# Kernel tuning notes

Hardware: AMD Instinct MI355X
Metric: run time of the kernel (lower is better)

Reference implementation:

```python
import jax, jax.numpy as jnp
import numpy as np

DIM = 2048
NUM_HEADS = 16
HEAD_DIM = DIM // NUM_HEADS
ROPE_BASE = 10000.0


def _rope_cos_sin(seq_len, head_dim, dtype):
    inv_freq = 1.0 / (ROPE_BASE ** (jnp.arange(0, head_dim, 2, dtype=jnp.float32) / head_dim))
    t = jnp.arange(seq_len, dtype=jnp.float32)
    freqs = jnp.einsum('i,j->ij', t, inv_freq)            # (T, head_dim/2)
    emb = jnp.concatenate([freqs, freqs], axis=-1)        # (T, head_dim)
    return jnp.cos(emb).astype(dtype), jnp.sin(emb).astype(dtype)


def _rotate_half(x):
    x1, x2 = jnp.split(x, 2, axis=-1)
    return jnp.concatenate([-x2, x1], axis=-1)


def setup_inputs() -> dict:
    key = jax.random.key(0)
    k1, k2, k3 = jax.random.split(key, 3)
    B, T = 2, 2048
    x = jax.random.normal(k1, (B, T, DIM), dtype=jnp.float32)
    # scale weights like nn.Linear default init (~1/sqrt(fan_in))
    w_qkv = jax.random.normal(k2, (DIM, 3 * DIM), dtype=jnp.float32) / np.sqrt(DIM)
    w_out = jax.random.normal(k3, (DIM, DIM), dtype=jnp.float32) / np.sqrt(DIM)
    return {"x": x, "w_qkv": w_qkv, "w_out": w_out}


def reference(x, w_qkv, w_out):
    B, T, D = x.shape
    H, Hd = NUM_HEADS, HEAD_DIM
    scale = Hd ** -0.5

    qkv = x @ w_qkv                                        # (B, T, 3D)
    q, k, v = jnp.split(qkv, 3, axis=-1)
    # (B, H, T, Hd)
    q = q.reshape(B, T, H, Hd).transpose(0, 2, 1, 3)
    k = k.reshape(B, T, H, Hd).transpose(0, 2, 1, 3)
    v = v.reshape(B, T, H, Hd).transpose(0, 2, 1, 3)

    cos, sin = _rope_cos_sin(T, Hd, x.dtype)               # (T, Hd)
    q = q * cos + _rotate_half(q) * sin
    k = k * cos + _rotate_half(k) * sin

    scores = jnp.einsum('bhqd,bhkd->bhqk', q, k) * scale   # (B, H, T, T)
    causal = jnp.tril(jnp.ones((T, T), dtype=bool))
    scores = jnp.where(causal[None, None, :, :], scores, jnp.float32(-jnp.inf))
    attn = jax.nn.softmax(scores, axis=-1)

    out = jnp.einsum('bhqk,bhkd->bhqd', attn, v)           # (B, H, T, Hd)
    out = out.transpose(0, 2, 1, 3).reshape(B, T, D)
    return out @ w_out
```

## Files before the change

kernel.cpp:

```cpp
#include <hip/hip_runtime.h>

typedef __attribute__((ext_vector_type(8))) short bf16x8;
typedef __attribute__((ext_vector_type(4))) float f32x4;

#define DEVICE __device__ __forceinline__

static constexpr int Tc = 2048;
static constexpr int Dc = 2048;
static constexpr int Hc = 16;
static constexpr int HD = 128;
static constexpr int MR = 4096;
static constexpr int NQKV = 6144;

DEVICE float bf2f(unsigned short u) {
  unsigned int t = ((unsigned int)u) << 16;
  float f; __builtin_memcpy(&f, &t, 4); return f;
}
DEVICE unsigned short f2bf(float f) {
  unsigned int t; __builtin_memcpy(&t, &f, 4);
  unsigned int r = (t + 0x7fffu + ((t >> 16) & 1u)) >> 16;
  return (unsigned short)r;
}

DEVICE void async_cp16(const void* g, void* lds) {
  __builtin_amdgcn_global_load_lds((const __attribute__((address_space(1))) void*)g,
                                   (__attribute__((address_space(3))) void*)lds, 16, 0, 0);
}

DEVICE int lsw(int t, int d2) {
  return t * 256 + (d2 ^ ((((t & 7) ^ ((t >> 3) & 7)) << 4)));
}

__global__ void rope_table_kernel(float2* cs) {
  int t = blockIdx.x;
  int j = threadIdx.x;
  float inv = powf(10000.0f, -(float)(2 * j) / 128.0f);
  float ang = (float)t * inv;
  cs[t * 64 + j] = make_float2(cosf(ang), sinf(ang));
}

__global__ void f32_to_bf16_kernel(const float* __restrict__ in,
                                   unsigned short* __restrict__ out, int n) {
  int i = (blockIdx.x * blockDim.x + threadIdx.x) * 4;
  if (i >= n) return;
  float4 v = *(const float4*)(in + i);
  ushort4 o;
  o.x = f2bf(v.x); o.y = f2bf(v.y); o.z = f2bf(v.z); o.w = f2bf(v.w);
  *(ushort4*)(out + i) = o;
}

__global__ __launch_bounds__(256)
void transpose_f32_bf16_kernel(const float* __restrict__ in,
                               unsigned short* __restrict__ out,
                               int R, int C) {
  __shared__ float tile[64][68];
  int c0 = blockIdx.x * 64, r0 = blockIdx.y * 64;
  int tid = threadIdx.x;
#pragma unroll
  for (int it = 0; it < 4; ++it) {
    int idx = it * 256 + tid;
    int r = idx >> 4;
    int c = (idx & 15) * 4;
    float4 v = *(const float4*)&in[(size_t)(r0 + r) * C + c0 + c];
    tile[r][c] = v.x; tile[r][c + 1] = v.y;
    tile[r][c + 2] = v.z; tile[r][c + 3] = v.w;
  }
  __syncthreads();
#pragma unroll
  for (int it = 0; it < 2; ++it) {
    int idx = it * 256 + tid;
    int r = idx >> 3;
    int c = (idx & 7) * 8;
    bf16x8 ov;
#pragma unroll
    for (int i = 0; i < 8; ++i) ov[i] = (short)f2bf(tile[c + i][r]);
    *(bf16x8*)&out[(size_t)(c0 + r) * R + r0 + c] = ov;
  }
}

__global__ __launch_bounds__(256, 2)
void gemm_qkv_kernel(const unsigned short* __restrict__ A,
                     const unsigned short* __restrict__ Bt,
                     const float2* __restrict__ cs,
                     unsigned short* __restrict__ qh,
                     unsigned short* __restrict__ kh,
                     unsigned short* __restrict__ vt) {
  const int N = NQKV, K = Dc;
  __shared__ __align__(16) unsigned short sh[128 * 128];
  unsigned short* As = sh;
  unsigned short* Bs = sh + 128 * 64;

  int nbx = N >> 7;
  int nwg = gridDim.x;
  int wg = blockIdx.x;
  int cpx = nwg >> 3;
  wg = (wg & 7) * cpx + (wg >> 3);
  int gsize = nbx * 8;
  int g = wg / gsize, rem = wg - g * gsize;
  int by = g * 8 + (rem & 7), bx = rem >> 3;
  int m0 = by << 7, n0 = bx << 7;

  int tid = threadIdx.x, lane = tid & 63, wid = tid >> 6;
  int wm = (wid >> 1) << 6, wn = (wid & 1) << 6;

  f32x4 acc[4][4] = {};

  for (int k0 = 0; k0 < K; k0 += 64) {
    __syncthreads();
#pragma unroll
    for (int r = 0; r < 4; ++r) {
      int p = r * 4096 + wid * 1024 + lane * 16;
      int row = p >> 7;
      int cb = (p & 127) ^ ((row & 7) << 4);
      const char* ga = (const char*)A + ((size_t)(m0 + row) * K + k0) * 2 + cb;
      async_cp16(ga, (char*)As + r * 4096 + wid * 1024);
      const char* gb = (const char*)Bt + ((size_t)(n0 + row) * K + k0) * 2 + cb;
      async_cp16(gb, (char*)Bs + r * 4096 + wid * 1024);
    }
    __syncthreads();

#pragma unroll
    for (int ks = 0; ks < 2; ++ks) {
      bf16x8 af[4], bfr[4];
#pragma unroll
      for (int mi = 0; mi < 4; ++mi) {
        int row = wm + mi * 16 + (lane & 15);
        int cb = (ks * 64 + ((lane >> 4) << 4)) ^ ((row & 7) << 4);
        af[mi] = *(const bf16x8*)((const char*)As + row * 128 + cb);
      }
#pragma unroll
      for (int ni = 0; ni < 4; ++ni) {
        int row = wn + ni * 16 + (lane & 15);
        int cb = (ks * 64 + ((lane >> 4) << 4)) ^ ((row & 7) << 4);
        bfr[ni] = *(const bf16x8*)((const char*)Bs + row * 128 + cb);
      }
#pragma unroll
      for (int mi = 0; mi < 4; ++mi)
#pragma unroll
        for (int ni = 0; ni < 4; ++ni)
          acc[mi][ni] = __builtin_amdgcn_mfma_f32_16x16x32_bf16(
              af[mi], bfr[ni], acc[mi][ni], 0, 0, 0);
    }
  }

  __syncthreads();
#pragma unroll
  for (int mi = 0; mi < 4; ++mi)
#pragma unroll
    for (int ni = 0; ni < 4; ++ni)
#pragma unroll
      for (int r = 0; r < 4; ++r) {
        int t_ = wm + mi * 16 + ((lane >> 4) << 2) + r;
        int d_ = wn + ni * 16 + (lane & 15);
        *(unsigned short*)((char*)sh + lsw(t_, d_ * 2)) = f2bf(acc[mi][ni][r]);
      }
  __syncthreads();

  int sector = n0 >> 11;
  int h = (n0 & 2047) >> 7;
  if (sector < 2) {
    unsigned short* dst = sector ? kh : qh;
#pragma unroll
    for (int it = 0; it < 4; ++it) {
      int idx = it * 256 + tid;
      int r = idx >> 3, j0 = (idx & 7) * 8;
      int m = m0 + r;
      int t = m & (Tc - 1), b = m >> 11;
      bf16x8 o1, o2;
#pragma unroll
      for (int i = 0; i < 8; ++i) {
        float q1 = bf2f(*(const unsigned short*)((const char*)sh + lsw(r, (j0 + i) * 2)));
        float q2 = bf2f(*(const unsigned short*)((const char*)sh + lsw(r, (j0 + i + 64) * 2)));
        float2 c = cs[t * 64 + j0 + i];
        o1[i] = (short)f2bf(q1 * c.x - q2 * c.y);
        o2[i] = (short)f2bf(q2 * c.x + q1 * c.y);
      }
      size_t ob = ((size_t)(b * Hc + h) * Tc + t) * HD;
      *(bf16x8*)(dst + ob + j0) = o1;
      *(bf16x8*)(dst + ob + 64 + j0) = o2;
    }
  } else {
    int bh = (m0 >> 11) * Hc + h;
    int tb = m0 & (Tc - 1);
#pragma unroll
    for (int it = 0; it < 8; ++it) {
      int idx = it * 256 + tid;
      int d = idx >> 4, tc = idx & 15;
      bf16x8 o;
#pragma unroll
      for (int i = 0; i < 8; ++i)
        o[i] = (short)*(const unsigned short*)((const char*)sh + lsw(tc * 8 + i, d * 2));
      *(bf16x8*)(vt + (size_t)(bh * HD + d) * Tc + tb + tc * 8) = o;
    }
  }
}

__global__ __launch_bounds__(256, 2)
void gemm_bt_kernel(const unsigned short* __restrict__ A,
                    const unsigned short* __restrict__ Bt,
                    float* __restrict__ C, int M, int N, int K) {
  __shared__ unsigned short As[128 * 64];
  __shared__ unsigned short Bs[128 * 64];

  int nbx = N >> 7;
  int nwg = gridDim.x;
  int wg = blockIdx.x;
  int cpx = nwg >> 3;
  wg = (wg & 7) * cpx + (wg >> 3);
  int gsize = nbx * 8;
  int g = wg / gsize, rem = wg - g * gsize;
  int by = g * 8 + (rem & 7), bx = rem >> 3;
  int m0 = by << 7, n0 = bx << 7;

  int tid = threadIdx.x, lane = tid & 63, wid = tid >> 6;
  int wm = (wid >> 1) << 6, wn = (wid & 1) << 6;

  f32x4 acc[4][4] = {};

  for (int k0 = 0; k0 < K; k0 += 64) {
    __syncthreads();
#pragma unroll
    for (int r = 0; r < 4; ++r) {
      int p = r * 4096 + wid * 1024 + lane * 16;
      int row = p >> 7;
      int cb = (p & 127) ^ ((row & 7) << 4);
      const char* ga = (const char*)A + ((size_t)(m0 + row) * K + k0) * 2 + cb;
      async_cp16(ga, (char*)As + r * 4096 + wid * 1024);
      const char* gb = (const char*)Bt + ((size_t)(n0 + row) * K + k0) * 2 + cb;
      async_cp16(gb, (char*)Bs + r * 4096 + wid * 1024);
    }
    __syncthreads();

#pragma unroll
    for (int ks = 0; ks < 2; ++ks) {
      bf16x8 af[4], bfr[4];
#pragma unroll
      for (int mi = 0; mi < 4; ++mi) {
        int row = wm + mi * 16 + (lane & 15);
        int cb = (ks * 64 + ((lane >> 4) << 4)) ^ ((row & 7) << 4);
        af[mi] = *(const bf16x8*)((const char*)As + row * 128 + cb);
      }
#pragma unroll
      for (int ni = 0; ni < 4; ++ni) {
        int row = wn + ni * 16 + (lane & 15);
        int cb = (ks * 64 + ((lane >> 4) << 4)) ^ ((row & 7) << 4);
        bfr[ni] = *(const bf16x8*)((const char*)Bs + row * 128 + cb);
      }
#pragma unroll
      for (int mi = 0; mi < 4; ++mi)
#pragma unroll
        for (int ni = 0; ni < 4; ++ni)
          acc[mi][ni] = __builtin_amdgcn_mfma_f32_16x16x32_bf16(
              af[mi], bfr[ni], acc[mi][ni], 0, 0, 0);
    }
  }

#pragma unroll
  for (int mi = 0; mi < 4; ++mi)
#pragma unroll
    for (int ni = 0; ni < 4; ++ni)
#pragma unroll
      for (int r = 0; r < 4; ++r) {
        int row = m0 + wm + mi * 16 + ((lane >> 4) << 2) + r;
        int col = n0 + wn + ni * 16 + (lane & 15);
        C[(size_t)row * N + col] = acc[mi][ni][r];
      }
}

__global__ __launch_bounds__(512, 1)
void attn_kernel(const unsigned short* __restrict__ qh,
                 const unsigned short* __restrict__ kh,
                 const unsigned short* __restrict__ vt,
                 unsigned short* __restrict__ ao) {
  const float scale = 0.08838834764831845f;
  int pairp = blockIdx.x;
  int bh = blockIdx.y;
  int b = bh >> 4, h = bh & 15;

  __shared__ unsigned short Ks[2][64 * 128];
  __shared__ unsigned short Vs[2][128 * 64];
  __shared__ unsigned short Ps[8][16 * 64];

  int tid = threadIdx.x, lane = tid & 63, wid = tid >> 6;

  const unsigned short* Kg = kh + (size_t)bh * Tc * HD;
  const unsigned short* Vg = vt + (size_t)bh * HD * Tc;

  auto stage = [&](int kt, int buf) {
#pragma unroll
    for (int r = 0; r < 2; ++r) {
      int p = r * 8192 + wid * 1024 + lane * 16;
      {
        int row = p >> 8, cb = p & 255;
        const char* g = (const char*)Kg + ((size_t)(kt * 64 + row)) * 256 +
                        (cb ^ ((row & 7) << 4));
        async_cp16(g, (char*)&Ks[buf][0] + r * 8192 + wid * 1024);
      }
      {
        int d = p >> 7, cb = p & 127;
        const char* g = (const char*)Vg + (size_t)d * (Tc * 2) + kt * 128 +
                        (cb ^ ((d & 7) << 4));
        async_cp16(g, (char*)&Vs[buf][0] + r * 8192 + wid * 1024);
      }
    }
  };

#pragma unroll 1
  for (int pass = 0; pass < 2; ++pass) {
    int qt = pass ? (15 - pairp) : pairp;
    const unsigned short* Qg = qh + ((size_t)bh * Tc + qt * 128) * HD;

    bf16x8 qf[4];
#pragma unroll
    for (int ks = 0; ks < 4; ++ks) {
      int row = wid * 16 + (lane & 15);
      qf[ks] = *(const bf16x8*)((const char*)Qg + row * 256 + ks * 64 +
                                ((lane >> 4) << 4));
    }

    f32x4 oacc[8] = {};
    float mrow[4], lrow[4];
#pragma unroll
    for (int r = 0; r < 4; ++r) { mrow[r] = -1e30f; lrow[r] = 0.f; }

    int nkt = 2 * (qt + 1);
    __syncthreads();
    stage(0, 0);
    int cur = 0;
#pragma unroll 1
    for (int kt = 0; kt < nkt; ++kt) {
      __syncthreads();
      if (kt + 1 < nkt) stage(kt + 1, cur ^ 1);

      f32x4 sacc[4] = {};
      __builtin_amdgcn_s_setprio(1);
#pragma unroll
      for (int ks = 0; ks < 4; ++ks) {
#pragma unroll
        for (int ni = 0; ni < 4; ++ni) {
          int row = ni * 16 + (lane & 15);
          int cb = (ks * 64 + ((lane >> 4) << 4)) ^ ((row & 7) << 4);
          bf16x8 kf = *(const bf16x8*)((const char*)&Ks[cur][0] + row * 256 + cb);
          sacc[ni] = __builtin_amdgcn_mfma_f32_16x16x32_bf16(qf[ks], kf,
                                                             sacc[ni], 0, 0, 0);
        }
      }
      __builtin_amdgcn_s_setprio(0);

      bool diag = (kt >= 2 * qt);
      float pvv[4][4];
      float fsc[4];
#pragma unroll
      for (int r = 0; r < 4; ++r) {
        int qrow = qt * 128 + wid * 16 + ((lane >> 4) << 2) + r;
        float sv[4];
        float mx = -1e30f;
#pragma unroll
        for (int ni = 0; ni < 4; ++ni) {
          float s = sacc[ni][r] * scale;
          if (diag) {
            int kcol = kt * 64 + ni * 16 + (lane & 15);
            if (kcol > qrow) s = -1e30f;
          }
          sv[ni] = s;
          mx = fmaxf(mx, s);
        }
        mx = fmaxf(mx, __shfl_xor(mx, 1));
        mx = fmaxf(mx, __shfl_xor(mx, 2));
        mx = fmaxf(mx, __shfl_xor(mx, 4));
        mx = fmaxf(mx, __shfl_xor(mx, 8));
        float mnew = fmaxf(mrow[r], mx);
        float f = __expf(mrow[r] - mnew);
        mrow[r] = mnew;
        float ls = 0.f;
#pragma unroll
        for (int ni = 0; ni < 4; ++ni) {
          float pp = __expf(sv[ni] - mnew);
          pvv[ni][r] = pp;
          ls += pp;
        }
        ls += __shfl_xor(ls, 1);
        ls += __shfl_xor(ls, 2);
        ls += __shfl_xor(ls, 4);
        ls += __shfl_xor(ls, 8);
        lrow[r] = lrow[r] * f + ls;
        fsc[r] = f;
      }
      bool need = (fsc[0] < 1.f) | (fsc[1] < 1.f) | (fsc[2] < 1.f) | (fsc[3] < 1.f);
      if (__any(need)) {
#pragma unroll
        for (int nj = 0; nj < 8; ++nj)
#pragma unroll
          for (int r = 0; r < 4; ++r) oacc[nj][r] *= fsc[r];
      }

#pragma unroll
      for (int ni = 0; ni < 4; ++ni)
#pragma unroll
        for (int r = 0; r < 4; ++r) {
          int row = ((lane >> 4) << 2) + r;
          int colb = (ni * 16 + (lane & 15)) * 2;
          *(unsigned short*)((char*)&Ps[wid][0] + row * 128 +
                             (colb ^ ((row & 7) << 4))) = f2bf(pvv[ni][r]);
        }

      __builtin_amdgcn_s_setprio(1);
#pragma unroll
      for (int ks = 0; ks < 2; ++ks) {
        int prow = lane & 15;
        int pcb = (ks * 64 + ((lane >> 4) << 4)) ^ ((prow & 7) << 4);
        bf16x8 pf = *(const bf16x8*)((const char*)&Ps[wid][0] + prow * 128 + pcb);
#pragma unroll
        for (int nj = 0; nj < 8; ++nj) {
          int vrow = nj * 16 + (lane & 15);
          int vcb = (ks * 64 + ((lane >> 4) << 4)) ^ ((vrow & 7) << 4);
          bf16x8 vf = *(const bf16x8*)((const char*)&Vs[cur][0] + vrow * 128 + vcb);
          oacc[nj] = __builtin_amdgcn_mfma_f32_16x16x32_bf16(pf, vf,
                                                             oacc[nj], 0, 0, 0);
        }
      }
      __builtin_amdgcn_s_setprio(0);
      cur ^= 1;
    }

    float inv[4];
#pragma unroll
    for (int r = 0; r < 4; ++r) inv[r] = 1.f / lrow[r];
#pragma unroll
    for (int nj = 0; nj < 8; ++nj)
#pragma unroll
      for (int r = 0; r < 4; ++r) {
        int trow = qt * 128 + wid * 16 + ((lane >> 4) << 2) + r;
        int col = nj * 16 + (lane & 15);
        ao[((size_t)(b * Tc + trow)) * Dc + h * HD + col] =
            f2bf(oacc[nj][r] * inv[r]);
      }
  }
}

extern "C" void kernel_launch(void* const* d_in, const int* in_sizes, int n_in,
                              void* d_out, int out_size, void* d_ws,
                              size_t ws_size, hipStream_t stream) {
  const float* x = (const float*)d_in[0];
  const float* w_qkv = (const float*)d_in[1];
  const float* w_out = (const float*)d_in[2];
  float* out = (float*)d_out;

  char* ws = (char*)d_ws;
  size_t off = 0;
  auto alloc = [&](size_t bytes) {
    char* p = ws + off;
    off += (bytes + 255) & ~(size_t)255;
    return p;
  };
  unsigned short* xb    = (unsigned short*)alloc((size_t)MR * Dc * 2);
  unsigned short* wqkvT = (unsigned short*)alloc((size_t)NQKV * Dc * 2);
  unsigned short* woutT = (unsigned short*)alloc((size_t)Dc * Dc * 2);
  unsigned short* qhp   = (unsigned short*)alloc((size_t)MR * Dc * 2);
  unsigned short* khp   = (unsigned short*)alloc((size_t)MR * Dc * 2);
  unsigned short* vtp   = (unsigned short*)alloc((size_t)MR * Dc * 2);
  unsigned short* aop   = (unsigned short*)alloc((size_t)MR * Dc * 2);
  float2* cs            = (float2*)alloc((size_t)Tc * 64 * sizeof(float2));

  rope_table_kernel<<<Tc, 64, 0, stream>>>(cs);
  f32_to_bf16_kernel<<<(MR * Dc / 4 + 255) / 256, 256, 0, stream>>>(x, xb, MR * Dc);
  transpose_f32_bf16_kernel<<<dim3(NQKV / 64, Dc / 64), 256, 0, stream>>>(
      w_qkv, wqkvT, Dc, NQKV);
  transpose_f32_bf16_kernel<<<dim3(Dc / 64, Dc / 64), 256, 0, stream>>>(
      w_out, woutT, Dc, Dc);
  gemm_qkv_kernel<<<(MR / 128) * (NQKV / 128), 256, 0, stream>>>(
      xb, wqkvT, cs, qhp, khp, vtp);
  attn_kernel<<<dim3(8, 32), 512, 0, stream>>>(qhp, khp, vtp, aop);
  gemm_bt_kernel<<<(MR / 128) * (Dc / 128), 256, 0, stream>>>(
      aop, woutT, out, MR, Dc, Dc);
}
```

Measured before the change: 267.9 us.

## Use lazy softmax rescaling with exp2 and deferred row-sum reduction

Folds log2(e) into the score scale so exp2f replaces __expf. The running max is only updated, with cross-lane shuffles and accumulator rescaling, when some row's tile max exceeds the stored max by more than a threshold of 8. Per-lane partial row sums are kept and reduced across lanes once at the end instead of every tile. This removes most shuffles and rescale work from the inner loop, but allows probabilities up to 2^8 before bf16 conversion, which risks some precision loss.

```diff
diff --git a/kernel.cpp b/kernel.cpp
--- a/kernel.cpp
+++ b/kernel.cpp
@@ -272,7 +272,7 @@
                  const unsigned short* __restrict__ kh,
                  const unsigned short* __restrict__ vt,
                  unsigned short* __restrict__ ao) {
-  const float scale = 0.08838834764831845f;
+  const float SCL2 = 0.08838834764831845f * 1.4426950408889634f;
   int pairp = blockIdx.x;
   int bh = blockIdx.y;
   int b = bh >> 4, h = bh & 15;
@@ -348,60 +348,53 @@
       __builtin_amdgcn_s_setprio(0);
 
       bool diag = (kt >= 2 * qt);
-      float pvv[4][4];
-      float fsc[4];
+      float sv[4][4];
+      float pmax[4];
+      bool allok = true;
 #pragma unroll
       for (int r = 0; r < 4; ++r) {
         int qrow = qt * 128 + wid * 16 + ((lane >> 4) << 2) + r;
-        float sv[4];
         float mx = -1e30f;
 #pragma unroll
         for (int ni = 0; ni < 4; ++ni) {
-          float s = sacc[ni][r] * scale;
+          float s = sacc[ni][r] * SCL2;
           if (diag) {
             int kcol = kt * 64 + ni * 16 + (lane & 15);
             if (kcol > qrow) s = -1e30f;
           }
-          sv[ni] = s;
+          sv[ni][r] = s;
           mx = fmaxf(mx, s);
         }
-        mx = fmaxf(mx, __shfl_xor(mx, 1));
-        mx = fmaxf(mx, __shfl_xor(mx, 2));
-        mx = fmaxf(mx, __shfl_xor(mx, 4));
-        mx = fmaxf(mx, __shfl_xor(mx, 8));
-        float mnew = fmaxf(mrow[r], mx);
-        float f = __expf(mrow[r] - mnew);
-        mrow[r] = mnew;
-        float ls = 0.f;
-#pragma unroll
-        for (int ni = 0; ni < 4; ++ni) {
-          float pp = __expf(sv[ni] - mnew);
-          pvv[ni][r] = pp;
-          ls += pp;
+        pmax[r] = mx;
+        allok = allok && (mx <= mrow[r] + 8.f);
+      }
+      if (!__all(allok)) {
+#pragma unroll
+        for (int r = 0; r < 4; ++r) {
+          float gm = pmax[r];
+          gm = fmaxf(gm, __shfl_xor(gm, 1));
+          gm = fmaxf(gm, __shfl_xor(gm, 2));
+          gm = fmaxf(gm, __shfl_xor(gm, 4));
+          gm = fmaxf(gm, __shfl_xor(gm, 8));
+          float mnew = fmaxf(mrow[r], gm);
+          float fsc = exp2f(mrow[r] - mnew);
+          mrow[r] = mnew;
+          lrow[r] *= fsc;
+#pragma unroll
+          for (int nj = 0; nj < 8; ++nj) oacc[nj][r] *= fsc;
         }
-        ls += __shfl_xor(ls, 1);
-        ls += __shfl_xor(ls, 2);
-        ls += __shfl_xor(ls, 4);
-        ls += __shfl_xor(ls, 8);
-        lrow[r] = lrow[r] * f + ls;
-        fsc[r] = f;
-      }
-      bool need = (fsc[0] < 1.f) | (fsc[1] < 1.f) | (fsc[2] < 1.f) | (fsc[3] < 1.f);
-      if (__any(need)) {
-#pragma unroll
-        for (int nj = 0; nj < 8; ++nj)
-#pragma unroll
-          for (int r = 0; r < 4; ++r) oacc[nj][r] *= fsc[r];
       }
 
 #pragma unroll
       for (int ni = 0; ni < 4; ++ni)
 #pragma unroll
         for (int r = 0; r < 4; ++r) {
+          float pp = exp2f(sv[ni][r] - mrow[r]);
+          lrow[r] += pp;
           int row = ((lane >> 4) << 2) + r;
           int colb = (ni * 16 + (lane & 15)) * 2;
           *(unsigned short*)((char*)&Ps[wid][0] + row * 128 +
-                             (colb ^ ((row & 7) << 4))) = f2bf(pvv[ni][r]);
+                             (colb ^ ((row & 7) << 4))) = f2bf(pp);
         }
 
       __builtin_amdgcn_s_setprio(1);
@@ -425,7 +418,14 @@
 
     float inv[4];
 #pragma unroll
-    for (int r = 0; r < 4; ++r) inv[r] = 1.f / lrow[r];
+    for (int r = 0; r < 4; ++r) {
+      float s = lrow[r];
+      s += __shfl_xor(s, 1);
+      s += __shfl_xor(s, 2);
+      s += __shfl_xor(s, 4);
+      s += __shfl_xor(s, 8);
+      inv[r] = 1.f / s;
+    }
 #pragma unroll
     for (int nj = 0; nj < 8; ++nj)
 #pragma unroll
```

Result: faster. 256.5 us (-4.3%).
